# Kernel optimization log

Measured on AMD Instinct MI355X. Metric: run time of the kernel, lower is better.

Reference implementation:

```python
import jax, jax.numpy as jnp
import numpy as np

C0 = 1.0  # speed of sound (units absorbed; distances pre-scaled)
FS = 1.0  # sampling frequency

A, E, S = 4, 128, 3072   # n_angles, n_elements, n_samples
NZ, NX = 512, 256        # image grid


def setup_inputs() -> dict:
    key = jax.random.key(0)
    k1, k2, k3, k4 = jax.random.split(key, 4)
    scale = (S / 2.0) - 1.0  # spread delays over the valid sample range
    d_tx = jax.random.uniform(k1, (A, NZ, NX), dtype=jnp.float32) * scale
    d_rx = jax.random.uniform(k2, (E, NZ, NX), dtype=jnp.float32) * scale
    apod = jax.random.uniform(k3, (E, NZ, NX), dtype=jnp.float32)
    rf = jax.random.normal(k4, (A, E, S), dtype=jnp.float32)
    t0 = jnp.zeros((A,), dtype=jnp.float32)
    return {"d_tx": d_tx, "d_rx": d_rx, "apod": apod, "rf": rf, "t0": t0}


def reference(d_tx, d_rx, apod, rf, t0):
    a, e, s = rf.shape
    nz, nx = d_tx.shape[1], d_tx.shape[2]
    # total delay in samples: [A, E, nz, nx]
    delays = ((d_tx[:, None] + d_rx[None]) / C0 - t0[:, None, None, None]) * FS
    x0 = jnp.floor(delays)
    w = delays - x0                      # linear interp weight
    i0 = x0.astype(jnp.int32)
    i1 = i0 + 1

    def gather(idx):
        # rf: [A, E, S]; idx: [A, E, nz, nx] -> gathered [A, E, nz, nx]
        g = jnp.take_along_axis(rf, jnp.clip(idx, 0, s - 1).reshape(a, e, -1), axis=2)
        return g.reshape(a, e, nz, nx)

    # grid_sample(padding_mode='zeros', align_corners=True): out-of-range taps contribute 0
    v0 = jnp.where((i0 >= 0) & (i0 <= s - 1), gather(i0), 0.0)
    v1 = jnp.where((i1 >= 0) & (i1 <= s - 1), gather(i1), 0.0)
    sampled = v0 * (1.0 - w) + v1 * w    # [A, E, nz, nx]
    # apodization-weighted sum over elements -> [A, nz, nx]
    das = jnp.einsum('aezx,ezx->azx', sampled, apod)
    return das
```

## Files before the change

kernel.cpp:

```cpp
#include <hip/hip_runtime.h>


#define A_N 4
#define E_N 128
#define S_N 3072
#define NPIX_N (512 * 256)
#define TPB 512
#define PXT 8
#define TILE (TPB * PXT)
#define TILES (NPIX_N / TILE)
#define ESPLIT 8
#define EPB (E_N / ESPLIT)
#define CPA (S_N / 256)
#define CHUNKS (A_N * CPA)
#define WAVES (TPB / 64)
#define CPW (CHUNKS / WAVES)

__device__ __forceinline__ void ld_lds16(const float* g, float* l) {
    __builtin_amdgcn_global_load_lds(
        (const __attribute__((address_space(1))) void*)g,
        (__attribute__((address_space(3))) void*)l, 16, 0, 0);
}

__global__ __launch_bounds__(TPB, 2) void das_kernel(
    const float* __restrict__ d_tx, const float* __restrict__ d_rx,
    const float* __restrict__ apod, const float* __restrict__ rf,
    const float* __restrict__ t0,  float* __restrict__ out)
{
    __shared__ float lds_rf[2][A_N * S_N];
    const int tid  = threadIdx.x;
    const int wid  = tid >> 6;
    const int lane = tid & 63;
    const int px0  = blockIdx.x * TILE + tid;
    const int e0   = blockIdx.y * EPB;

    auto stage = [&](int b, int e) {
#pragma unroll
        for (int j = 0; j < CPW; ++j) {
            const int chunk = wid * CPW + j;
            const int a = chunk / CPA;
            const int c = chunk - a * CPA;
            const float* g = rf + ((size_t)(a * E_N + e)) * S_N + c * 256 + lane * 4;
            float* l = &lds_rf[b][a * S_N + c * 256];
            ld_lds16(g, l);
        }
    };

    stage(0, e0);

    float acc[A_N][PXT];
    float dta[A_N][PXT];
#pragma unroll
    for (int a = 0; a < A_N; ++a) {
        const float t0a = t0[a];
#pragma unroll
        for (int k = 0; k < PXT; ++k) {
            dta[a][k] = d_tx[a * NPIX_N + px0 + k * TPB] - t0a;
            acc[a][k] = 0.0f;
        }
    }

    __syncthreads();

    for (int ei = 0; ei < EPB; ++ei) {
        const int e   = e0 + ei;
        const int cur = ei & 1;

        if (ei + 1 < EPB) stage(cur ^ 1, e + 1);

        const float* __restrict__ drx_row = d_rx + (size_t)e * NPIX_N;
        const float* __restrict__ ap_row  = apod + (size_t)e * NPIX_N;
        const float* __restrict__ L = lds_rf[cur];

#pragma unroll
        for (int k = 0; k < PXT; ++k) {
            const int p = px0 + k * TPB;
            const float drx = drx_row[p];
            const float ap  = ap_row[p];
#pragma unroll
            for (int a = 0; a < A_N; ++a) {
                float delay = dta[a][k] + drx;
                float x0 = floorf(delay);
                float w  = delay - x0;
                int i0 = (int)x0;
                i0 = min(max(i0, 0), S_N - 2);
                float v0 = L[a * S_N + i0];
                float v1 = L[a * S_N + i0 + 1];
                acc[a][k] += (v0 + w * (v1 - v0)) * ap;
            }
        }

        __syncthreads();
    }

#pragma unroll
    for (int a = 0; a < A_N; ++a)
#pragma unroll
        for (int k = 0; k < PXT; ++k)
            atomicAdd(&out[a * NPIX_N + px0 + k * TPB], acc[a][k]);
}

extern "C" void kernel_launch(void* const* d_in, const int* in_sizes, int n_in,
                              void* d_out, int out_size, void* d_ws, size_t ws_size,
                              hipStream_t stream) {
    const float* d_tx = (const float*)d_in[0];
    const float* d_rx = (const float*)d_in[1];
    const float* apod = (const float*)d_in[2];
    const float* rf   = (const float*)d_in[3];
    const float* t0   = (const float*)d_in[4];
    float* out = (float*)d_out;

    hipMemsetAsync(out, 0, (size_t)out_size * sizeof(float), stream);
    dim3 grid(TILES, ESPLIT);
    das_kernel<<<grid, TPB, 0, stream>>>(d_tx, d_rx, apod, rf, t0, out);
}
```

Before: 194.0 us.

## Prefetch next element's d_rx/apod into registers and use 1024-thread blocks

Loads the next element's receive delay and apodization values into registers during the current element's iteration, so global-load latency overlaps the LDS interpolation work. Block size doubles to 1024 threads with half as many pixels per thread, keeping the tile size fixed, and the launch-bounds min-blocks hint is removed. The larger block shares each rf stage among more waves but allows fewer blocks per CU given the 96KB of LDS double buffer. It also changes per-thread register pressure.

```diff
diff --git a/kernel.cpp b/kernel.cpp
--- a/kernel.cpp
+++ b/kernel.cpp
@@ -5,8 +5,8 @@
 #define E_N 128
 #define S_N 3072
 #define NPIX_N (512 * 256)
-#define TPB 512
-#define PXT 8
+#define TPB 1024
+#define PXT 4
 #define TILE (TPB * PXT)
 #define TILES (NPIX_N / TILE)
 #define ESPLIT 8
@@ -22,7 +22,7 @@
         (__attribute__((address_space(3))) void*)l, 16, 0, 0);
 }
 
-__global__ __launch_bounds__(TPB, 2) void das_kernel(
+__global__ __launch_bounds__(TPB) void das_kernel(
     const float* __restrict__ d_tx, const float* __restrict__ d_rx,
     const float* __restrict__ apod, const float* __restrict__ rf,
     const float* __restrict__ t0,  float* __restrict__ out)
@@ -60,33 +60,47 @@
         }
     }
 
+    float ndrx[PXT], nap[PXT];
+#pragma unroll
+    for (int k = 0; k < PXT; ++k) {
+        ndrx[k] = d_rx[(size_t)e0 * NPIX_N + px0 + k * TPB];
+        nap[k]  = apod[(size_t)e0 * NPIX_N + px0 + k * TPB];
+    }
+
     __syncthreads();
 
     for (int ei = 0; ei < EPB; ++ei) {
         const int e   = e0 + ei;
         const int cur = ei & 1;
 
-        if (ei + 1 < EPB) stage(cur ^ 1, e + 1);
+        float drx[PXT], ap[PXT];
+#pragma unroll
+        for (int k = 0; k < PXT; ++k) { drx[k] = ndrx[k]; ap[k] = nap[k]; }
 
-        const float* __restrict__ drx_row = d_rx + (size_t)e * NPIX_N;
-        const float* __restrict__ ap_row  = apod + (size_t)e * NPIX_N;
+        if (ei + 1 < EPB) {
+            stage(cur ^ 1, e + 1);
+            const float* __restrict__ nd = d_rx + (size_t)(e + 1) * NPIX_N;
+            const float* __restrict__ na = apod + (size_t)(e + 1) * NPIX_N;
+#pragma unroll
+            for (int k = 0; k < PXT; ++k) {
+                ndrx[k] = nd[px0 + k * TPB];
+                nap[k]  = na[px0 + k * TPB];
+            }
+        }
+
         const float* __restrict__ L = lds_rf[cur];
-
 #pragma unroll
         for (int k = 0; k < PXT; ++k) {
-            const int p = px0 + k * TPB;
-            const float drx = drx_row[p];
-            const float ap  = ap_row[p];
 #pragma unroll
             for (int a = 0; a < A_N; ++a) {
-                float delay = dta[a][k] + drx;
+                float delay = dta[a][k] + drx[k];
                 float x0 = floorf(delay);
                 float w  = delay - x0;
                 int i0 = (int)x0;
                 i0 = min(max(i0, 0), S_N - 2);
                 float v0 = L[a * S_N + i0];
                 float v1 = L[a * S_N + i0 + 1];
-                acc[a][k] += (v0 + w * (v1 - v0)) * ap;
+                acc[a][k] += (v0 + w * (v1 - v0)) * ap[k];
             }
         }
 
```

Result: faster. 180.9 us (-6.8%).
